# Kernel tuning notes

Measured on AMD Instinct MI355X. Metric: run time of the kernel, lower is better.

Reference implementation:

```python
import jax, jax.numpy as jnp
import numpy as np

L, H, NH, KVH, HD, F, P, DLM, N = 4, 1024, 16, 2, 64, 4096, 4, 2048, 8192
QLEN = P + 1  # patch_size + 1 (special token prepended)
EPS = 1e-5


def _rms(x, w):
    return x * jax.lax.rsqrt(jnp.mean(x * x, axis=-1, keepdims=True) + EPS) * w


def _rotate_half(x):
    x1, x2 = jnp.split(x, 2, axis=-1)  # split_size = head_dim // 2
    return jnp.concatenate([-x2, x1], axis=-1)


def _rope_tables():
    pos = jnp.arange(QLEN, dtype=jnp.float32)
    inv_freq = 1.0 / (10000.0 ** (jnp.arange(0, HD, 2, dtype=jnp.float32) / HD))
    freqs = pos[:, None] * inv_freq[None, :]
    emb = jnp.concatenate([freqs, freqs], axis=-1)  # [QLEN, HD]
    scale = HD ** -0.25  # scale_factor baked into cos/sin as in source
    return jnp.cos(emb) * scale, jnp.sin(emb) * scale


def setup_inputs() -> dict:
    key = jax.random.key(0)
    ks = jax.random.split(key, 12)
    s = 0.02
    return {
        "audio_feat": jax.random.normal(ks[0], (N, P, 64), jnp.float32),
        "special_token": jax.random.normal(ks[1], (H,), jnp.float32) * s,
        "in_proj_w": jax.random.normal(ks[2], (64, H), jnp.float32) * s,
        "ln1_w": jnp.ones((L, H), jnp.float32),
        "wq": jax.random.normal(ks[3], (L, H, NH * HD), jnp.float32) * s,
        "wk": jax.random.normal(ks[4], (L, H, KVH * HD), jnp.float32) * s,
        "wv": jax.random.normal(ks[5], (L, H, KVH * HD), jnp.float32) * s,
        "wo": jax.random.normal(ks[6], (L, NH * HD, H), jnp.float32) * s,
        "ln2_w": jnp.ones((L, H), jnp.float32),
        "w_gate": jax.random.normal(ks[7], (L, H, F), jnp.float32) * s,
        "w_up": jax.random.normal(ks[8], (L, H, F), jnp.float32) * s,
        "w_down": jax.random.normal(ks[9], (L, F, H), jnp.float32) * s,
        "final_norm_w": jnp.ones((H,), jnp.float32),
        "enc_to_lm_w": jax.random.normal(ks[10], (H, DLM), jnp.float32) * s,
    }


def reference(audio_feat, special_token, in_proj_w, ln1_w, wq, wk, wv, wo,
              ln2_w, w_gate, w_up, w_down, final_norm_w, enc_to_lm_w):
    n = audio_feat.shape[0]
    h = audio_feat @ in_proj_w  # [N, P, H]
    sp = jnp.broadcast_to(special_token, (n, 1, H))
    h = jnp.concatenate([sp, h], axis=1)  # [N, QLEN, H]
    cos, sin = _rope_tables()
    g = NH // KVH  # num_key_value_groups
    for l in range(L):
        x = _rms(h, ln1_w[l])
        q = (x @ wq[l]).reshape(n, QLEN, NH, HD).transpose(0, 2, 1, 3)
        k = (x @ wk[l]).reshape(n, QLEN, KVH, HD).transpose(0, 2, 1, 3)
        v = (x @ wv[l]).reshape(n, QLEN, KVH, HD).transpose(0, 2, 1, 3)
        q = q * cos + _rotate_half(q) * sin
        k = k * cos + _rotate_half(k) * sin
        # explicit GQA repeat (cat-then-view == repeat along head axis)
        k = jnp.repeat(k, g, axis=1)
        v = jnp.repeat(v, g, axis=1)
        attn = jax.nn.softmax(jnp.einsum('bhqd,bhkd->bhqk', q, k), axis=-1)
        ao = jnp.einsum('bhqk,bhkd->bhqd', attn, v)
        ao = ao.transpose(0, 2, 1, 3).reshape(n, QLEN, NH * HD)
        h = h + ao @ wo[l]
        r = h
        x = _rms(h, ln2_w[l])
        h = r + (jax.nn.silu(x @ w_gate[l]) * (x @ w_up[l])) @ w_down[l]
    feat = _rms(h[:, 0], final_norm_w) @ enc_to_lm_w  # [N, DLM]
    return feat[None]  # [1, N, DLM]
```

## Files before the change

kernel.cpp:

```cpp
#include <hip/hip_runtime.h>
#include <hip/hip_bf16.h>

#define NSAMP 8192
#define QL 5
#define MTOK (NSAMP*QL)

typedef __hip_bfloat16 bf16;
typedef __attribute__((ext_vector_type(8))) __bf16 bf16x8;
typedef __attribute__((ext_vector_type(8))) unsigned short u16x8;
typedef __attribute__((ext_vector_type(4))) float f32x4;

__device__ __forceinline__ float bfu2f(unsigned short u){ return __uint_as_float(((unsigned)u)<<16); }
__device__ __forceinline__ float bf2f(bf16 v){ return __bfloat162float(v); }
__device__ __forceinline__ bf16  f2bf(float v){ return __float2bfloat16(v); }
__device__ __forceinline__ unsigned short f2bfu(float v){
  __hip_bfloat16 b = __float2bfloat16(v);
  return __builtin_bit_cast(unsigned short, b);
}

__device__ __forceinline__ void gload16(const void* g, void* l){
  __builtin_amdgcn_global_load_lds(
      (const __attribute__((address_space(1))) unsigned int*)g,
      (__attribute__((address_space(3))) unsigned int*)l, 16, 0, 0);
}

template<int RMAP>
__global__ __launch_bounds__(256) void k_transpose_cvt(const float* __restrict__ in,
                                                       bf16* __restrict__ out,
                                                       int K, int N){
  __shared__ float tile[32][33];
  int nb = blockIdx.x*32, kb = blockIdx.y*32;
  int tx = threadIdx.x, ty = threadIdx.y;
  #pragma unroll
  for (int j=0;j<4;j++)
    tile[ty+8*j][tx] = in[(size_t)(kb+ty+8*j)*N + nb+tx];
  __syncthreads();
  #pragma unroll
  for (int j=0;j<4;j++){
    int n = nb+ty+8*j;
    int R = (RMAP==0) ? n : (((n>>4)<<5) + (n&15) + (RMAP==2 ? 16 : 0));
    out[(size_t)R*K + kb+tx] = f2bf(tile[tx][ty+8*j]);
  }
}

__global__ __launch_bounds__(256) void k_cvt_bf16(const float* __restrict__ in,
                                                  bf16* __restrict__ out, int n4){
  int i = blockIdx.x*blockDim.x + threadIdx.x;
  if (i < n4){
    float4 v = ((const float4*)in)[i];
    out[4*i+0]=f2bf(v.x); out[4*i+1]=f2bf(v.y);
    out[4*i+2]=f2bf(v.z); out[4*i+3]=f2bf(v.w);
  }
}

__global__ __launch_bounds__(256) void k_fill_special(const float* __restrict__ sp,
                                                      bf16* __restrict__ h){
  int i = blockIdx.x*blockDim.x + threadIdx.x;
  int n = i >> 10, c = i & 1023;
  h[(size_t)n*QL*1024 + c] = f2bf(sp[c]);
}

__global__ void k_rope_tab(float* __restrict__ ctab, float* __restrict__ stab){
  int i = threadIdx.x;
  int t = i >> 6, d = i & 63, j = d & 31;
  float invf = __expf(-((float)j/32.0f) * logf(10000.0f));
  float ang  = (float)t * invf;
  const float s = 0.35355339059327373f;
  ctab[i] = cosf(ang)*s;
  stab[i] = sinf(ang)*s;
}

__global__ __launch_bounds__(256) void k_rmsnorm(const bf16* __restrict__ in,
                                                 const float* __restrict__ w,
                                                 bf16* __restrict__ out,
                                                 int nrows, int in_stride){
  int row  = blockIdx.x*4 + (threadIdx.x>>6);
  int lane = threadIdx.x & 63;
  if (row >= nrows) return;
  const bf16* p = in + (size_t)row*in_stride;
  float f[16]; float ss = 0.f;
  #pragma unroll
  for (int i=0;i<2;i++){
    u16x8 v = *(const u16x8*)(p + i*512 + lane*8);
    #pragma unroll
    for (int j=0;j<8;j++){ float x = bfu2f(v[j]); f[i*8+j] = x; ss += x*x; }
  }
  #pragma unroll
  for (int off=32; off; off>>=1) ss += __shfl_xor(ss, off);
  float inv = rsqrtf(ss * (1.0f/1024.0f) + 1e-5f);
  const float4* w4 = (const float4*)w;
  bf16* op = out + (size_t)row*1024;
  #pragma unroll
  for (int i=0;i<2;i++){
    int c = i*512 + lane*8;
    float4 wa = w4[c/4], wb = w4[c/4 + 1];
    u16x8 o;
    o[0]=f2bfu(f[i*8+0]*inv*wa.x); o[1]=f2bfu(f[i*8+1]*inv*wa.y);
    o[2]=f2bfu(f[i*8+2]*inv*wa.z); o[3]=f2bfu(f[i*8+3]*inv*wa.w);
    o[4]=f2bfu(f[i*8+4]*inv*wb.x); o[5]=f2bfu(f[i*8+5]*inv*wb.y);
    o[6]=f2bfu(f[i*8+6]*inv*wb.z); o[7]=f2bfu(f[i*8+7]*inv*wb.w);
    *(u16x8*)(op + c) = o;
  }
}

template<int OUTMODE>
__global__ __launch_bounds__(512) void k_gemm256(const bf16* __restrict__ A,
                                                 const bf16* __restrict__ B,
                                                 float* __restrict__ Cf,
                                                 bf16* __restrict__ Cb,
                                                 int M, int N, int K, int ldc){
  __shared__ bf16 lds[65536];
  char* ldsb = (char*)lds;
  const int tid  = threadIdx.x;
  const int wid  = tid >> 6, lane = tid & 63;
  const int wr   = wid >> 2, wc  = wid & 3;
  const int fr   = lane & 15, fq = lane >> 4;
  const int swz = (fr & 7) << 4;
  const int cs0 = (fq*16) ^ swz;
  const int cs1 = (fq*16 + 64) ^ swz;
  const int srcR = lane >> 3;
  const int srcC = ((lane & 7) ^ srcR) * 8;

  const int bm0 = blockIdx.x*256, bn0 = blockIdx.y*256;
  const bf16* gA = A + (size_t)bm0*K;
  const bf16* gB = B + (size_t)bn0*K;
  const int nt = K >> 6;

  const int aOff = (wr ? 16384 : 0);
  const int bOff = 32768 + ((wc>>1) ? 16384 : 0) + (wc&1)*8192;
  const char* aB0 = ldsb + aOff + fr*128 + cs0;
  const char* aB1 = ldsb + aOff + fr*128 + cs1;
  const char* bB0 = ldsb + bOff + fr*128 + cs0;
  const char* bB1 = ldsb + bOff + fr*128 + cs1;

  f32x4 acc[8][4] = {};
  bf16x8 aF[8][2], bF[4][2];

#define STAGE(p, t, h) {                                                        \
    const bf16* G_ = ((h) < 2) ? gA : gB;                                       \
    const int rb_ = ((h)&1) ? 128 : 0;                                          \
    const int k0_ = (t) << 6;                                                   \
    _Pragma("unroll")                                                           \
    for (int j_=0;j_<2;j_++){                                                   \
      int blk_ = j_*8 + wid;                                                    \
      gload16(G_ + (size_t)(rb_ + blk_*8 + srcR)*K + k0_ + srcC,               \
              ldsb + (p)*65536 + (h)*16384 + blk_*1024);                        \
    }                                                                           \
  }
#define RD_A(p, m0_) {                                                          \
    _Pragma("unroll")                                                           \
    for (int m_=0;m_<4;m_++)                                                    \
      _Pragma("unroll")                                                         \
      for (int ks_=0;ks_<2;ks_++)                                               \
        aF[(m0_)+m_][ks_] = *(const bf16x8*)((ks_ ? aB1 : aB0) + (p)*65536 + ((m0_)+m_)*2048); \
  }
#define RD_B(p, n0_) {                                                          \
    _Pragma("unroll")                                                           \
    for (int n_=0;n_<2;n_++)                                                    \
      _Pragma("unroll")                                                         \
      for (int ks_=0;ks_<2;ks_++)                                               \
        bF[(n0_)+n_][ks_] = *(const bf16x8*)((ks_ ? bB1 : bB0) + (p)*65536 + ((n0_)+n_)*2048); \
  }
#define MM(qm_, qn_) {                                                          \
    _Pragma("unroll")                                                           \
    for (int m_=0;m_<4;m_++)                                                    \
      _Pragma("unroll")                                                         \
      for (int n_=0;n_<2;n_++)                                                  \
        _Pragma("unroll")                                                       \
        for (int ks_=0;ks_<2;ks_++)                                             \
          acc[(qm_)*4+m_][(qn_)*2+n_] = __builtin_amdgcn_mfma_f32_16x16x32_bf16( \
              aF[(qm_)*4+m_][ks_], bF[(qn_)*2+n_][ks_], acc[(qm_)*4+m_][(qn_)*2+n_], 0,0,0); \
  }
#define LGKM0  asm volatile("s_waitcnt lgkmcnt(0)" ::: "memory"); __builtin_amdgcn_sched_barrier(0)
#define BAR    __builtin_amdgcn_s_barrier()

  STAGE(0, 0, 0); STAGE(0, 0, 1); STAGE(0, 0, 2); STAGE(0, 0, 3);
  if (nt > 1){ STAGE(1, 1, 0); STAGE(1, 1, 1); STAGE(1, 1, 2); STAGE(1, 1, 3); }
  if (nt > 1) asm volatile("s_waitcnt vmcnt(8)" ::: "memory");
  else        asm volatile("s_waitcnt vmcnt(0)" ::: "memory");
  BAR;

  for (int t = 0; t < nt; t++){
    const int cur = t & 1;
    const bool pf = (t + 2) < nt;
    RD_A(cur, 0); RD_B(cur, 0);
    BAR; LGKM0;
    __builtin_amdgcn_s_setprio(1); MM(0,0); __builtin_amdgcn_s_setprio(0);
    BAR;
    RD_A(cur, 4);
    BAR; LGKM0;
    __builtin_amdgcn_s_setprio(1); MM(1,0); __builtin_amdgcn_s_setprio(0);
    BAR;
    RD_B(cur, 2);
    if (pf) STAGE(cur, t+2, 0);
    BAR; LGKM0;
    __builtin_amdgcn_s_setprio(1); MM(0,1); __builtin_amdgcn_s_setprio(0);
    BAR;
    if (pf){ STAGE(cur, t+2, 1); STAGE(cur, t+2, 2); STAGE(cur, t+2, 3); }
    BAR;
    __builtin_amdgcn_s_setprio(1); MM(1,1); __builtin_amdgcn_s_setprio(0);
    if (t + 1 < nt){
      if (pf) asm volatile("s_waitcnt vmcnt(8)" ::: "memory");
      else    asm volatile("s_waitcnt vmcnt(0)" ::: "memory");
    }
    BAR;
  }

  #pragma unroll
  for (int m=0;m<8;m++){
    if constexpr (OUTMODE == 2){
      #pragma unroll
      for (int n2=0;n2<2;n2++){
        #pragma unroll
        for (int i=0;i<4;i++){
          int row = bm0 + wr*128 + m*16 + fq*4 + i;
          int col = (bn0>>1) + wc*32 + n2*16 + fr;
          float g = acc[m][n2*2][i], u = acc[m][n2*2+1][i];
          Cb[(size_t)row*ldc + col] = f2bf((g / (1.0f + __expf(-g))) * u);
        }
      }
    } else {
      #pragma unroll
      for (int n=0;n<4;n++){
        #pragma unroll
        for (int i=0;i<4;i++){
          int row = bm0 + wr*128 + m*16 + fq*4 + i;
          int col = bn0 + wc*64 + n*16 + fr;
          size_t idx = (size_t)row*ldc + col;
          if constexpr (OUTMODE == 0)      Cf[idx] = acc[m][n][i];
          else if constexpr (OUTMODE == 1) Cb[idx] = f2bf(acc[m][n][i]);
          else                             Cb[idx] = f2bf(bf2f(Cb[idx]) + acc[m][n][i]);
        }
      }
    }
  }
#undef STAGE
#undef RD_A
#undef RD_B
#undef MM
#undef LGKM0
#undef BAR
}

__global__ __launch_bounds__(256) void k_gemm_embed(const bf16* __restrict__ A,
                                                    const bf16* __restrict__ B0,
                                                    bf16* __restrict__ Cb,
                                                    int M, int N, int K, int ldc){
  constexpr int BM = 128, BN = 128, BK = 32;
  constexpr int WN = BN/2, NR = WN/16, MR = 4;
  __shared__ bf16 lA[BM*BK];
  __shared__ bf16 lB[BN*BK];
  int wid = threadIdx.x >> 6, lane = threadIdx.x & 63;
  int wr = wid >> 1, wc = wid & 1;
  int bm0 = blockIdx.x * BM, bn0 = blockIdx.y * BN;
  int fr = lane & 15, fq = lane >> 4;
  int rowInCh = lane >> 2, colInCh = (lane & 3)*8;
  f32x4 acc[MR][NR] = {};
  const bf16* gA = A + (size_t)bm0*K;
  const bf16* gB = B0 + (size_t)bn0*K;
  for (int k0 = 0; k0 < K; k0 += BK){
    #pragma unroll
    for (int i = 0; i < BM/64; i++){
      int ch = wid + 4*i;
      gload16(gA + (size_t)(16*ch + rowInCh)*K + k0 + colInCh, lA + 16*ch*BK);
    }
    #pragma unroll
    for (int i = 0; i < BN/64; i++){
      int ch = wid + 4*i;
      gload16(gB + (size_t)(16*ch + rowInCh)*K + k0 + colInCh, lB + 16*ch*BK);
    }
    __syncthreads();
    bf16x8 af[MR];
    #pragma unroll
    for (int m=0;m<MR;m++)
      af[m] = *(const bf16x8*)(lA + (wr*64 + m*16 + fr)*BK + fq*8);
    #pragma unroll
    for (int n=0;n<NR;n++){
      bf16x8 bfr = *(const bf16x8*)(lB + (wc*WN + n*16 + fr)*BK + fq*8);
      #pragma unroll
      for (int m=0;m<MR;m++)
        acc[m][n] = __builtin_amdgcn_mfma_f32_16x16x32_bf16(af[m], bfr, acc[m][n], 0,0,0);
    }
    __syncthreads();
  }
  #pragma unroll
  for (int m=0;m<MR;m++)
    #pragma unroll
    for (int n=0;n<NR;n++)
      #pragma unroll
      for (int i=0;i<4;i++){
        int row = bm0 + wr*64 + m*16 + fq*4 + i;
        int col = bn0 + wc*WN + n*16 + fr;
        size_t orow = (size_t)(row + (row>>2) + 1);
        Cb[orow*(size_t)ldc + col] = f2bf(acc[m][n][i]);
      }
}

__global__ __launch_bounds__(256) void k_attn(const bf16* __restrict__ qkv,
                                              bf16* __restrict__ xn,
                                              const float* __restrict__ ctab,
                                              const float* __restrict__ stab){
  int gw   = blockIdx.x*4 + (threadIdx.x>>6);
  int lane = threadIdx.x & 63;
  int sample = gw >> 4, head = gw & 15, kvh = head >> 3;

  float qf[QL], kf[QL], vf[QL];
  #pragma unroll
  for (int t=0;t<QL;t++){
    size_t r = (size_t)(sample*QL + t)*1280;
    qf[t] = bf2f(qkv[r + head*64 + lane]);
    kf[t] = bf2f(qkv[r + 1024 + kvh*64 + lane]);
    vf[t] = bf2f(qkv[r + 1152 + kvh*64 + lane]);
  }
  #pragma unroll
  for (int t=0;t<QL;t++){
    float c = ctab[t*64+lane], s = stab[t*64+lane];
    float qo = __shfl_xor(qf[t], 32);
    float ko = __shfl_xor(kf[t], 32);
    float rq = (lane < 32) ? -qo : qo;
    float rk = (lane < 32) ? -ko : ko;
    qf[t] = qf[t]*c + rq*s;
    kf[t] = kf[t]*c + rk*s;
  }
  float p[QL][QL];
  #pragma unroll
  for (int i=0;i<QL;i++)
    #pragma unroll
    for (int j=0;j<QL;j++) p[i][j] = qf[i]*kf[j];
  #pragma unroll
  for (int off=32; off; off>>=1){
    #pragma unroll
    for (int i=0;i<QL;i++)
      #pragma unroll
      for (int j=0;j<QL;j++) p[i][j] += __shfl_xor(p[i][j], off);
  }
  #pragma unroll
  for (int i=0;i<QL;i++){
    float mx = p[i][0];
    #pragma unroll
    for (int j=1;j<QL;j++) mx = fmaxf(mx, p[i][j]);
    float sum = 0.f;
    #pragma unroll
    for (int j=0;j<QL;j++){ p[i][j] = __expf(p[i][j]-mx); sum += p[i][j]; }
    float rs = 1.0f/sum;
    float o = 0.f;
    #pragma unroll
    for (int j=0;j<QL;j++) o += p[i][j]*vf[j];
    xn[((size_t)(sample*QL+i))*1024 + head*64 + lane] = f2bf(o*rs);
  }
}

__global__ void k_diag(float* out, float v){ out[0] = v; }

extern "C" void kernel_launch(void* const* d_in, const int* in_sizes, int n_in,
                              void* d_out, int out_size, void* d_ws, size_t ws_size,
                              hipStream_t stream){
  const float* audio = (const float*)d_in[0];
  const float* sp    = (const float*)d_in[1];
  const float* inpw  = (const float*)d_in[2];
  const float* ln1   = (const float*)d_in[3];
  const float* wq    = (const float*)d_in[4];
  const float* wk    = (const float*)d_in[5];
  const float* wv    = (const float*)d_in[6];
  const float* wo    = (const float*)d_in[7];
  const float* ln2   = (const float*)d_in[8];
  const float* wg    = (const float*)d_in[9];
  const float* wu    = (const float*)d_in[10];
  const float* wd    = (const float*)d_in[11];
  const float* fnw   = (const float*)d_in[12];
  const float* enc   = (const float*)d_in[13];
  float* out = (float*)d_out;
  char* ws = (char*)d_ws;

  size_t o_h=0,o_wqkv=0,o_wo=0,o_wgu=0,o_wd=0,o_ct=0,o_st=0,o_xn=0,o_u=0;
  size_t CH=0, RM=0;
  const size_t tiers[4] = {8192, 4096, 2048, 1024};
  for (int t=0;t<4;t++){
    size_t ch = tiers[t], R = ch*QL, rm = (ch==8192) ? 20480 : R/2;
    size_t off = 0;
    auto al = [&](size_t b){ size_t o=off; off=(off+b+255)&~(size_t)255; return o; };
    o_h   = al((size_t)MTOK*1024*2);
    o_wqkv= al((size_t)1280*1024*2);
    o_wo  = al((size_t)1024*1024*2);
    o_wgu = al((size_t)8192*1024*2);
    o_wd  = al((size_t)1024*4096*2);
    o_ct  = al(QL*64*4);
    o_st  = al(QL*64*4);
    o_xn  = al(R*1024*2);
    size_t qkvB = R*1280*2, actB = rm*4096*2;
    o_u   = al(qkvB > actB ? qkvB : actB);
    if (off <= ws_size){ CH = ch; RM = rm; break; }
  }
  if (CH == 0){ k_diag<<<1,1,0,stream>>>(out, (float)ws_size); return; }
  const size_t R = CH*QL;

  bf16*  h     = (bf16*)(ws + o_h);
  bf16*  wqkvT = (bf16*)(ws + o_wqkv);
  bf16*  woT   = (bf16*)(ws + o_wo);
  bf16*  wguT  = (bf16*)(ws + o_wgu);
  bf16*  wdT   = (bf16*)(ws + o_wd);
  float* ctab  = (float*)(ws + o_ct);
  float* stab  = (float*)(ws + o_st);
  bf16*  xn    = (bf16*)(ws + o_xn);
  bf16*  qkv   = (bf16*)(ws + o_u);
  bf16*  act   = (bf16*)(ws + o_u);
  bf16*  af16  = (bf16*)(ws + o_u);
  bf16*  inprojT = wqkvT;
  bf16*  encT    = wguT;

  dim3 tb(32,8);
  k_rope_tab<<<1, 320, 0, stream>>>(ctab, stab);
  k_transpose_cvt<0><<<dim3(32, 2), tb, 0, stream>>>(inpw, inprojT, 64, 1024);
  k_cvt_bf16<<<(32768*64/4)/256, 256, 0, stream>>>(audio, af16, 32768*64/4);
  k_fill_special<<<NSAMP*1024/256, 256, 0, stream>>>(sp, h);
  k_gemm_embed<<<dim3(32768/128, 1024/128), 256, 0, stream>>>(
      af16, inprojT, h, 32768, 1024, 64, 1024);

  for (int l=0;l<4;l++){
    k_transpose_cvt<0><<<dim3(32, 32), tb, 0, stream>>>(wq + (size_t)l*1024*1024, wqkvT, 1024, 1024);
    k_transpose_cvt<0><<<dim3(4, 32),  tb, 0, stream>>>(wk + (size_t)l*1024*128,  wqkvT + (size_t)1024*1024, 1024, 128);
    k_transpose_cvt<0><<<dim3(4, 32),  tb, 0, stream>>>(wv + (size_t)l*1024*128,  wqkvT + (size_t)1152*1024, 1024, 128);
    k_transpose_cvt<0><<<dim3(32, 32), tb, 0, stream>>>(wo + (size_t)l*1024*1024, woT, 1024, 1024);
    k_transpose_cvt<1><<<dim3(128,32), tb, 0, stream>>>(wg + (size_t)l*1024*4096, wguT, 1024, 4096);
    k_transpose_cvt<2><<<dim3(128,32), tb, 0, stream>>>(wu + (size_t)l*1024*4096, wguT, 1024, 4096);
    k_transpose_cvt<0><<<dim3(32,128), tb, 0, stream>>>(wd + (size_t)l*4096*1024, wdT, 4096, 1024);

    for (size_t c0 = 0; c0 < NSAMP; c0 += CH){
      size_t r0 = c0*QL;
      k_rmsnorm<<<R/4, 256, 0, stream>>>(h + r0*1024, ln1 + l*1024, xn, (int)R, 1024);
      k_gemm256<1><<<dim3(R/256, 5), 512, 0, stream>>>(
          xn, wqkvT, nullptr, qkv, (int)R, 1280, 1024, 1280);
      k_attn<<<CH*16/4, 256, 0, stream>>>(qkv, xn, ctab, stab);
      k_gemm256<3><<<dim3(R/256, 4), 512, 0, stream>>>(
          xn, woT, nullptr, h + r0*1024, (int)R, 1024, 1024, 1024);
      k_rmsnorm<<<R/4, 256, 0, stream>>>(h + r0*1024, ln2 + l*1024, xn, (int)R, 1024);
      for (size_t m0 = 0; m0 < R; m0 += RM){
        k_gemm256<2><<<dim3(RM/256, 32), 512, 0, stream>>>(
            xn + m0*1024, wguT, nullptr, act, (int)RM, 8192, 1024, 4096);
        k_gemm256<3><<<dim3(RM/256, 4), 512, 0, stream>>>(
            act, wdT, nullptr, h + (r0+m0)*1024, (int)RM, 1024, 4096, 1024);
      }
    }
  }

  k_transpose_cvt<0><<<dim3(64, 32), tb, 0, stream>>>(enc, encT, 1024, 2048);
  for (size_t c0 = 0; c0 < NSAMP; c0 += CH){
    k_rmsnorm<<<CH/4, 256, 0, stream>>>(h + c0*QL*1024, fnw, xn, (int)CH, QL*1024);
    k_gemm256<0><<<dim3(CH/256, 2048/256), 512, 0, stream>>>(
        xn, encT, out + c0*2048, nullptr, (int)CH, 2048, 1024, 2048);
  }
}
```

Before: 7.368 ms.

## Fuse residual adds into RMSNorm and run full-batch MLP when workspace allows

Adds a k_addnorm kernel that adds the residual branch to h, writes h back, and emits the normalized activations in one pass. This lets the Wo and down-projection GEMM epilogues do plain stores instead of scalar read-modify-write accumulation into h. A new workspace tier processes all 40960 tokens in single GEMM launches without splitting the MLP, reducing launch count. GEMM variants get separate kernel names. The fused path only runs if the workspace fits the largest tier; otherwise the old chunked path is kept.

```diff
diff --git a/kernel.cpp b/kernel.cpp
--- a/kernel.cpp
+++ b/kernel.cpp
@@ -103,12 +103,64 @@
   }
 }
 
+template<bool WRITEH>
+__global__ __launch_bounds__(256) void k_addnorm(bf16* __restrict__ h,
+                                                 const float* __restrict__ w,
+                                                 const bf16* add,
+                                                 bf16* out,
+                                                 int nrows, int in_stride){
+  int row  = blockIdx.x*4 + (threadIdx.x>>6);
+  int lane = threadIdx.x & 63;
+  if (row >= nrows) return;
+  bf16* hp = h + (size_t)row*in_stride;
+  const bf16* ap = add + (size_t)row*in_stride;
+  float f[16]; float ss = 0.f;
+  u16x8 hv[2], av[2];
+  #pragma unroll
+  for (int i=0;i<2;i++){
+    hv[i] = *(const u16x8*)(hp + i*512 + lane*8);
+    av[i] = *(const u16x8*)(ap + i*512 + lane*8);
+  }
+  #pragma unroll
+  for (int i=0;i<2;i++)
+    #pragma unroll
+    for (int j=0;j<8;j++){
+      float x = bfu2f(hv[i][j]) + bfu2f(av[i][j]);
+      f[i*8+j] = x; ss += x*x;
+    }
+  if constexpr (WRITEH){
+    #pragma unroll
+    for (int i=0;i<2;i++){
+      u16x8 o;
+      #pragma unroll
+      for (int j=0;j<8;j++) o[j] = f2bfu(f[i*8+j]);
+      *(u16x8*)(hp + i*512 + lane*8) = o;
+    }
+  }
+  #pragma unroll
+  for (int off=32; off; off>>=1) ss += __shfl_xor(ss, off);
+  float inv = rsqrtf(ss * (1.0f/1024.0f) + 1e-5f);
+  const float4* w4 = (const float4*)w;
+  bf16* op = out + (size_t)row*1024;
+  #pragma unroll
+  for (int i=0;i<2;i++){
+    int c = i*512 + lane*8;
+    float4 wa = w4[c/4], wb = w4[c/4 + 1];
+    u16x8 o;
+    o[0]=f2bfu(f[i*8+0]*inv*wa.x); o[1]=f2bfu(f[i*8+1]*inv*wa.y);
+    o[2]=f2bfu(f[i*8+2]*inv*wa.z); o[3]=f2bfu(f[i*8+3]*inv*wa.w);
+    o[4]=f2bfu(f[i*8+4]*inv*wb.x); o[5]=f2bfu(f[i*8+5]*inv*wb.y);
+    o[6]=f2bfu(f[i*8+6]*inv*wb.z); o[7]=f2bfu(f[i*8+7]*inv*wb.w);
+    *(u16x8*)(op + c) = o;
+  }
+}
+
 template<int OUTMODE>
-__global__ __launch_bounds__(512) void k_gemm256(const bf16* __restrict__ A,
-                                                 const bf16* __restrict__ B,
-                                                 float* __restrict__ Cf,
-                                                 bf16* __restrict__ Cb,
-                                                 int M, int N, int K, int ldc){
+__device__ __forceinline__ void gemm256_impl(const bf16* __restrict__ A,
+                                             const bf16* __restrict__ B,
+                                             float* __restrict__ Cf,
+                                             bf16* __restrict__ Cb,
+                                             int M, int N, int K, int ldc){
   __shared__ bf16 lds[65536];
   char* ldsb = (char*)lds;
   const int tid  = threadIdx.x;
@@ -242,6 +294,28 @@
 #undef BAR
 }
 
+__global__ __launch_bounds__(512) void k_gemm_qkv(const bf16* A, const bf16* B, bf16* Cb, int M, int N, int K, int ldc){
+  gemm256_impl<1>(A, B, nullptr, Cb, M, N, K, ldc);
+}
+__global__ __launch_bounds__(512) void k_gemm_wo(const bf16* A, const bf16* B, bf16* Cb, int M, int N, int K, int ldc){
+  gemm256_impl<1>(A, B, nullptr, Cb, M, N, K, ldc);
+}
+__global__ __launch_bounds__(512) void k_gemm_gu(const bf16* A, const bf16* B, bf16* Cb, int M, int N, int K, int ldc){
+  gemm256_impl<2>(A, B, nullptr, Cb, M, N, K, ldc);
+}
+__global__ __launch_bounds__(512) void k_gemm_down(const bf16* A, const bf16* B, bf16* Cb, int M, int N, int K, int ldc){
+  gemm256_impl<1>(A, B, nullptr, Cb, M, N, K, ldc);
+}
+__global__ __launch_bounds__(512) void k_gemm_out(const bf16* A, const bf16* B, float* Cf, int M, int N, int K, int ldc){
+  gemm256_impl<0>(A, B, Cf, nullptr, M, N, K, ldc);
+}
+__global__ __launch_bounds__(512) void k_gemm_wo_acc(const bf16* A, const bf16* B, bf16* Cb, int M, int N, int K, int ldc){
+  gemm256_impl<3>(A, B, nullptr, Cb, M, N, K, ldc);
+}
+__global__ __launch_bounds__(512) void k_gemm_down_acc(const bf16* A, const bf16* B, bf16* Cb, int M, int N, int K, int ldc){
+  gemm256_impl<3>(A, B, nullptr, Cb, M, N, K, ldc);
+}
+
 __global__ __launch_bounds__(256) void k_gemm_embed(const bf16* __restrict__ A,
                                                     const bf16* __restrict__ B0,
                                                     bf16* __restrict__ Cb,
@@ -374,9 +448,10 @@
 
   size_t o_h=0,o_wqkv=0,o_wo=0,o_wgu=0,o_wd=0,o_ct=0,o_st=0,o_xn=0,o_u=0;
   size_t CH=0, RM=0;
-  const size_t tiers[4] = {8192, 4096, 2048, 1024};
-  for (int t=0;t<4;t++){
-    size_t ch = tiers[t], R = ch*QL, rm = (ch==8192) ? 20480 : R/2;
+  const size_t tierCH[5] = {8192, 8192, 4096, 2048, 1024};
+  const size_t tierRM[5] = {40960, 20480, 10240, 5120, 2560};
+  for (int t=0;t<5;t++){
+    size_t ch = tierCH[t], R = ch*QL, rm = tierRM[t];
     size_t off = 0;
     auto al = [&](size_t b){ size_t o=off; off=(off+b+255)&~(size_t)255; return o; };
     o_h   = al((size_t)MTOK*1024*2);
@@ -404,6 +479,8 @@
   bf16*  xn    = (bf16*)(ws + o_xn);
   bf16*  qkv   = (bf16*)(ws + o_u);
   bf16*  act   = (bf16*)(ws + o_u);
+  bf16*  ao    = (bf16*)(ws + o_u);
+  bf16*  xc    = (bf16*)(ws + o_u);
   bf16*  af16  = (bf16*)(ws + o_u);
   bf16*  inprojT = wqkvT;
   bf16*  encT    = wguT;
@@ -425,28 +502,41 @@
     k_transpose_cvt<2><<<dim3(128,32), tb, 0, stream>>>(wu + (size_t)l*1024*4096, wguT, 1024, 4096);
     k_transpose_cvt<0><<<dim3(32,128), tb, 0, stream>>>(wd + (size_t)l*4096*1024, wdT, 4096, 1024);
 
+    if (CH == NSAMP){
+      if (l == 0)
+        k_rmsnorm<<<R/4, 256, 0, stream>>>(h, ln1 + l*1024, xn, (int)R, 1024);
+      else
+        k_addnorm<true><<<R/4, 256, 0, stream>>>(h, ln1 + l*1024, xn, xn, (int)R, 1024);
+      k_gemm_qkv<<<dim3(R/256, 5), 512, 0, stream>>>(xn, wqkvT, qkv, (int)R, 1280, 1024, 1280);
+      k_attn<<<CH*16/4, 256, 0, stream>>>(qkv, xn, ctab, stab);
+      k_gemm_wo<<<dim3(R/256, 4), 512, 0, stream>>>(xn, woT, ao, (int)R, 1024, 1024, 1024);
+      k_addnorm<true><<<R/4, 256, 0, stream>>>(h, ln2 + l*1024, ao, xn, (int)R, 1024);
+      k_gemm_gu<<<dim3(R/256, 32), 512, 0, stream>>>(xn, wguT, act, (int)R, 8192, 1024, 4096);
+      k_gemm_down<<<dim3(R/256, 4), 512, 0, stream>>>(act, wdT, xn, (int)R, 1024, 4096, 1024);
+    } else {
+      for (size_t c0 = 0; c0 < NSAMP; c0 += CH){
+        size_t r0 = c0*QL;
+        k_rmsnorm<<<R/4, 256, 0, stream>>>(h + r0*1024, ln1 + l*1024, xn, (int)R, 1024);
+        k_gemm_qkv<<<dim3(R/256, 5), 512, 0, stream>>>(xn, wqkvT, qkv, (int)R, 1280, 1024, 1280);
+        k_attn<<<CH*16/4, 256, 0, stream>>>(qkv, xn, ctab, stab);
+        k_gemm_wo_acc<<<dim3(R/256, 4), 512, 0, stream>>>(xn, woT, h + r0*1024, (int)R, 1024, 1024, 1024);
+        k_rmsnorm<<<R/4, 256, 0, stream>>>(h + r0*1024, ln2 + l*1024, xn, (int)R, 1024);
+        for (size_t m0 = 0; m0 < R; m0 += RM){
+          k_gemm_gu<<<dim3(RM/256, 32), 512, 0, stream>>>(xn + m0*1024, wguT, act, (int)RM, 8192, 1024, 4096);
+          k_gemm_down_acc<<<dim3(RM/256, 4), 512, 0, stream>>>(act, wdT, h + (r0+m0)*1024, (int)RM, 1024, 4096, 1024);
+        }
+      }
+    }
+  }
+
+  k_transpose_cvt<0><<<dim3(64, 32), tb, 0, stream>>>(enc, encT, 1024, 2048);
+  if (CH == NSAMP){
+    k_addnorm<false><<<NSAMP/4, 256, 0, stream>>>(h, fnw, xn, xc, NSAMP, QL*1024);
+    k_gemm_out<<<dim3(NSAMP/256, 2048/256), 512, 0, stream>>>(xc, encT, out, NSAMP, 2048, 1024, 2048);
+  } else {
     for (size_t c0 = 0; c0 < NSAMP; c0 += CH){
-      size_t r0 = c0*QL;
-      k_rmsnorm<<<R/4, 256, 0, stream>>>(h + r0*1024, ln1 + l*1024, xn, (int)R, 1024);
-      k_gemm256<1><<<dim3(R/256, 5), 512, 0, stream>>>(
-          xn, wqkvT, nullptr, qkv, (int)R, 1280, 1024, 1280);
-      k_attn<<<CH*16/4, 256, 0, stream>>>(qkv, xn, ctab, stab);
-      k_gemm256<3><<<dim3(R/256, 4), 512, 0, stream>>>(
-          xn, woT, nullptr, h + r0*1024, (int)R, 1024, 1024, 1024);
-      k_rmsnorm<<<R/4, 256, 0, stream>>>(h + r0*1024, ln2 + l*1024, xn, (int)R, 1024);
-      for (size_t m0 = 0; m0 < R; m0 += RM){
-        k_gemm256<2><<<dim3(RM/256, 32), 512, 0, stream>>>(
-            xn + m0*1024, wguT, nullptr, act, (int)RM, 8192, 1024, 4096);
-        k_gemm256<3><<<dim3(RM/256, 4), 512, 0, stream>>>(
-            act, wdT, nullptr, h + (r0+m0)*1024, (int)RM, 1024, 4096, 1024);
-      }
-    }
-  }
-
-  k_transpose_cvt<0><<<dim3(64, 32), tb, 0, stream>>>(enc, encT, 1024, 2048);
-  for (size_t c0 = 0; c0 < NSAMP; c0 += CH){
-    k_rmsnorm<<<CH/4, 256, 0, stream>>>(h + c0*QL*1024, fnw, xn, (int)CH, QL*1024);
-    k_gemm256<0><<<dim3(CH/256, 2048/256), 512, 0, stream>>>(
-        xn, encT, out + c0*2048, nullptr, (int)CH, 2048, 1024, 2048);
-  }
-}
+      k_rmsnorm<<<CH/4, 256, 0, stream>>>(h + c0*QL*1024, fnw, xn, (int)CH, QL*1024);
+      k_gemm_out<<<dim3(CH/256, 2048/256), 512, 0, stream>>>(xn, encT, out + c0*2048, (int)CH, 2048, 1024, 2048);
+    }
+  }
+}
```

After: 7.372 ms. No clear change (+0.1%).
